# Performance work log

Hardware: AMD Instinct MI355X
Metric: run time of the kernel (lower is better)

## Reference

```python
import math
import jax, jax.numpy as jnp
import numpy as np

K = 64            # multiplicity per irrep
NE = 10           # num_elements
N_NODES = 10000
N_EDGES = 100000
AVG_NEIGH = 10.0
EDGE_DIM = 8
LS = [0, 1, 2]    # node/intermediate irreps 64x0e+64x1o+64x2e
LS_OUT = [0, 1]   # output irreps 64x0e+64x1o
INV_SQRT_K = 1.0 / math.sqrt(K)
MIX_NORM = 1.0 / math.sqrt(K * NE)

# ---- real spherical-harmonic Clebsch-Gordan coefficients (small l, exact) ----
def _cg(j1, m1, j2, m2, j3, m3):
    if m1 + m2 != m3 or not (abs(j1 - j2) <= j3 <= j1 + j2):
        return 0.0
    f = math.factorial
    pre = math.sqrt((2 * j3 + 1) * f(j1 + j2 - j3) * f(j1 - j2 + j3) * f(-j1 + j2 + j3) / f(j1 + j2 + j3 + 1))
    pre *= math.sqrt(f(j1 + m1) * f(j1 - m1) * f(j2 + m2) * f(j2 - m2) * f(j3 + m3) * f(j3 - m3))
    s = 0.0
    for k in range(j1 + j2 + j3 + 1):
        d = (j1 + j2 - j3 - k, j1 - m1 - k, j2 + m2 - k, j3 - j2 + m1 + k, j3 - j1 - m2 + k)
        if min(d) < 0:
            continue
        s += (-1) ** k / (f(k) * f(d[0]) * f(d[1]) * f(d[2]) * f(d[3]) * f(d[4]))
    return pre * s

def _u_real(l):
    # complex->real SH change of basis: Y_real = U @ Y_complex
    U = np.zeros((2 * l + 1, 2 * l + 1), dtype=np.complex128)
    U[l, l] = 1.0
    s = 1.0 / math.sqrt(2.0)
    for m in range(1, l + 1):
        U[l + m, l + m] = (-1) ** m * s
        U[l + m, l - m] = s
        U[l - m, l + m] = -1j * (-1) ** m * s
        U[l - m, l - m] = 1j * s
    return U

def real_cg(l1, l2, l3):
    C = np.zeros((2 * l1 + 1, 2 * l2 + 1, 2 * l3 + 1), dtype=np.complex128)
    for m1 in range(-l1, l1 + 1):
        for m2 in range(-l2, l2 + 1):
            m3 = m1 + m2
            if abs(m3) <= l3:
                C[l1 + m1, l2 + m2, l3 + m3] = _cg(l1, m1, l2, m2, l3, m3)
    U1, U2, U3 = _u_real(l1), _u_real(l2), _u_real(l3)
    Cr = np.einsum('ai,bj,ck,ijk->abc', U1, U2, U3.conj(), C)
    return np.ascontiguousarray(Cr.real).astype(np.float32)  # real since l1+l2+l3 even

# parity/triangle allowed paths (l1: edge sph, l2: node in, l3: intermediate) -> 11 paths
EDGE_PATHS = [(l1, l2, l3) for l1 in LS for l2 in LS for l3 in LS
              if abs(l1 - l2) <= l3 <= l1 + l2 and (l1 + l2 + l3) % 2 == 0]
N_EDGE_PATHS = len(EDGE_PATHS)  # 11
DEG2_PATHS = [(0, 0, 0), (1, 1, 0), (2, 2, 0), (0, 1, 1), (1, 2, 1)]
DEG3_PATHS = [(0, 0, 0), (1, 1, 0), (0, 1, 1), (1, 0, 1), (1, 2, 1)]
CG_EDGE = [real_cg(*p) for p in EDGE_PATHS]
CG_D2 = [real_cg(*p) for p in DEG2_PATHS]
CG_D3 = [real_cg(*p) for p in DEG3_PATHS]

def split_irreps(x, ls, mul):
    # ir_mul layout: per irrep a [(2l+1)*mul] flat segment, m index outer
    out, o = [], 0
    for l in ls:
        d = (2 * l + 1) * mul
        out.append(x[:, o:o + d].reshape(x.shape[0], 2 * l + 1, mul))
        o += d
    return out


def setup_inputs() -> dict:
    key = jax.random.key(0)
    ks = jax.random.split(key, 20)
    sender = jax.random.randint(ks[0], (N_EDGES,), 0, N_NODES)
    receiver = jax.random.randint(ks[1], (N_EDGES,), 0, N_NODES)
    indices = jax.random.randint(ks[2], (N_NODES,), 0, NE)
    node_attrs = jax.nn.one_hot(indices, NE, dtype=jnp.float32)
    node_feature_in = jax.random.normal(ks[3], (N_NODES, K * 9), dtype=jnp.float32)
    edge_length_embed = jax.random.normal(ks[4], (N_EDGES, EDGE_DIM), dtype=jnp.float32)
    edge_sph_embed = jax.random.normal(ks[5], (N_EDGES, 9), dtype=jnp.float32)
    W_lin_in = jax.random.normal(ks[6], (3, K, K), dtype=jnp.float32)
    mlp_W0 = jax.random.normal(ks[7], (EDGE_DIM, 32), dtype=jnp.float32) / math.sqrt(EDGE_DIM)
    mlp_b0 = jnp.zeros((32,), jnp.float32)
    mlp_W1 = jax.random.normal(ks[8], (32, 32), dtype=jnp.float32) / math.sqrt(32.0)
    mlp_b1 = jnp.zeros((32,), jnp.float32)
    mlp_W2 = jax.random.normal(ks[9], (32, 32), dtype=jnp.float32) / math.sqrt(32.0)
    mlp_b2 = jnp.zeros((32,), jnp.float32)
    mlp_W3 = jax.random.normal(ks[10], (32, N_EDGE_PATHS * K), dtype=jnp.float32) / math.sqrt(32.0)
    mlp_b3 = jnp.zeros((N_EDGE_PATHS * K,), jnp.float32)
    W_mix = jax.random.normal(ks[11], (3, NE, K, K), dtype=jnp.float32)
    w1 = jax.random.normal(ks[12], (NE, 2, K), dtype=jnp.float32)
    w2 = 0.1 * jax.random.normal(ks[13], (NE, len(DEG2_PATHS), K), dtype=jnp.float32)
    w3 = 0.05 * jax.random.normal(ks[14], (NE, len(DEG3_PATHS), K), dtype=jnp.float32)
    W_out_m = jax.random.normal(ks[15], (2, K, K), dtype=jnp.float32)
    W_out_h = jax.random.normal(ks[16], (2, K, K), dtype=jnp.float32)
    return dict(sender=sender, receiver=receiver, indices=indices, node_attrs=node_attrs,
                node_feature_in=node_feature_in, edge_length_embed=edge_length_embed,
                edge_sph_embed=edge_sph_embed, W_lin_in=W_lin_in,
                mlp_W0=mlp_W0, mlp_b0=mlp_b0, mlp_W1=mlp_W1, mlp_b1=mlp_b1,
                mlp_W2=mlp_W2, mlp_b2=mlp_b2, mlp_W3=mlp_W3, mlp_b3=mlp_b3,
                W_mix=W_mix, w1=w1, w2=w2, w3=w3, W_out_m=W_out_m, W_out_h=W_out_h)


def reference(sender, receiver, indices, node_attrs, node_feature_in,
              edge_length_embed, edge_sph_embed, W_lin_in,
              mlp_W0, mlp_b0, mlp_W1, mlp_b1, mlp_W2, mlp_b2, mlp_W3, mlp_b3,
              W_mix, w1, w2, w3, W_out_m, W_out_h):
    N = node_feature_in.shape[0]
    h1 = split_irreps(node_feature_in, LS, K)  # per-l [N, 2l+1, K]
    # ELinear_h1_2_h1p: per-irrep channel mixing
    h1p = [jnp.einsum('nmc,cd->nmd', h1[l], W_lin_in[l]) * INV_SQRT_K for l in LS]
    # residual radial MLP -> per-edge TP path weights [E, P, K]
    h = jax.nn.silu(edge_length_embed @ mlp_W0 + mlp_b0)
    h = h + jax.nn.silu(h @ mlp_W1 + mlp_b1)
    h = h + jax.nn.silu(h @ mlp_W2 + mlp_b2)
    Rl = (h @ mlp_W3 + mlp_b3).reshape(-1, N_EDGE_PATHS, K)
    sph = split_irreps(edge_sph_embed, LS, 1)  # per-l [E, 2l+1, 1]
    gx = [h1p[l][sender] for l in LS]          # gather sender node features
    # channelwise equivariant tensor product with per-edge radial weights
    msg = [None, None, None]
    for p, (l1, l2, l3) in enumerate(EDGE_PATHS):
        t = jnp.einsum('abd,ea,ebc->edc', jnp.asarray(CG_EDGE[p]), sph[l1][:, :, 0], gx[l2])
        t = t * Rl[:, p, None, :]
        msg[l3] = t if msg[l3] is None else msg[l3] + t
    # scatter-sum messages to receivers, normalized by avg num neighbors
    A = [jax.ops.segment_sum(msg[l], receiver, num_segments=N) / AVG_NEIGH for l in LS]
    # element-conditioned mixing (FCTP with num_elements x 0e attrs)
    Amix = [jnp.einsum('nmc,ne,ecd->nmd', A[l], node_attrs, W_mix[l]) * MIX_NORM for l in LS]
    # symmetric contraction (body order 3) with element-dependent channelwise weights
    w1n, w2n, w3n = w1[indices], w2[indices], w3[indices]
    T2 = [jnp.zeros_like(Amix[L]) for L in LS_OUT]
    for p, (l1, l2, L) in enumerate(DEG2_PATHS):
        t = jnp.einsum('abd,nac,nbc->ndc', jnp.asarray(CG_D2[p]), Amix[l1], Amix[l2])
        T2[L] = T2[L] + w2n[:, p, None, :] * t
    T3 = [jnp.zeros_like(Amix[L]) for L in LS_OUT]
    for q, (Lp, l3, L) in enumerate(DEG3_PATHS):
        t = jnp.einsum('abd,nac,nbc->ndc', jnp.asarray(CG_D3[q]), T2[Lp], Amix[l3])
        T3[L] = T3[L] + w3n[:, q, None, :] * t
    B = [w1n[:, L, None, :] * Amix[L] + T2[L] + T3[L] for L in LS_OUT]
    # node_feature_out = ELinear_h1_2_h2(h1) + ELinear_m2_2_h2(B)
    out = []
    for L in LS_OUT:
        y = jnp.einsum('nmc,cd->nmd', h1[L], W_out_h[L]) * INV_SQRT_K
        y = y + jnp.einsum('nmc,cd->nmd', B[L], W_out_m[L]) * INV_SQRT_K
        out.append(y.reshape(N, -1))
    return jnp.concatenate(out, axis=1)  # [N, 4K] = [N, 256]
```

## Files before the change

kernel.cpp:

```cpp
#include <hip/hip_runtime.h>
#include <math.h>

#define NNODES 10000
#define NEDGES 100000
#define EPW 8

struct Cplx { double re, im; };

constexpr double cfact(int n){ double r=1.0; for(int i=2;i<=n;++i) r*=i; return r; }

constexpr double csqrt_(double x){
  if (x<=0.0) return 0.0;
  double g = x<1.0 ? 1.0 : x;
  for (int it=0; it<64; ++it){ double ng = 0.5*(g + x/g); if (ng==g) break; g = ng; }
  return g;
}

constexpr double cg_coeff(int j1,int m1,int j2,int m2,int j3,int m3){
  if (m1+m2!=m3) return 0.0;
  int lo = j1>j2 ? j1-j2 : j2-j1;
  if (j3<lo || j3>j1+j2) return 0.0;
  if (m1<-j1||m1>j1||m2<-j2||m2>j2||m3<-j3||m3>j3) return 0.0;
  double pre = csqrt_((2.0*j3+1.0)*cfact(j1+j2-j3)*cfact(j1-j2+j3)*cfact(-j1+j2+j3)/cfact(j1+j2+j3+1));
  pre *= csqrt_(cfact(j1+m1)*cfact(j1-m1)*cfact(j2+m2)*cfact(j2-m2)*cfact(j3+m3)*cfact(j3-m3));
  double s = 0.0;
  for (int k=0;k<=j1+j2+j3;++k){
    int d0=j1+j2-j3-k, d1=j1-m1-k, d2=j2+m2-k, d3=j3-j2+m1+k, d4=j3-j1-m2+k;
    if (d0<0||d1<0||d2<0||d3<0||d4<0) continue;
    double term = 1.0/(cfact(k)*cfact(d0)*cfact(d1)*cfact(d2)*cfact(d3)*cfact(d4));
    s += (k&1) ? -term : term;
  }
  return pre*s;
}

constexpr Cplx uent(int l,int a,int i){
  const double s = 0.70710678118654752440;
  int ma = a - l;
  if (ma==0) { if (i==l) return Cplx{1.0,0.0}; return Cplx{0.0,0.0}; }
  if (ma>0){
    int m = ma; double sg = (m&1) ? -1.0 : 1.0;
    if (i==l+m) return Cplx{sg*s, 0.0};
    if (i==l-m) return Cplx{s, 0.0};
    return Cplx{0.0,0.0};
  }
  int m = -ma; double sg = (m&1) ? -1.0 : 1.0;
  if (i==l+m) return Cplx{0.0, -sg*s};
  if (i==l-m) return Cplx{0.0, s};
  return Cplx{0.0,0.0};
}

constexpr double real_cg_entry(int l1,int l2,int l3,int a,int b,int c){
  double acc = 0.0;
  int ii0 = a, ii1 = 2*l1-a;
  int jj0 = b, jj1 = 2*l2-b;
  for (int x=0;x<2;++x){
    int i = (x==0)? ii0 : ii1;
    if (x==1 && ii1==ii0) break;
    Cplx u1 = uent(l1,a,i); if (u1.re==0.0 && u1.im==0.0) continue;
    for (int y=0;y<2;++y){
      int j = (y==0)? jj0 : jj1;
      if (y==1 && jj1==jj0) break;
      Cplx u2 = uent(l2,b,j); if (u2.re==0.0 && u2.im==0.0) continue;
      int k = (i-l1)+(j-l2)+l3;
      if (k<0 || k>2*l3) continue;
      Cplx u3 = uent(l3,c,k); if (u3.re==0.0 && u3.im==0.0) continue;
      double cg = cg_coeff(l1,i-l1,l2,j-l2,l3,k-l3);
      if (cg==0.0) continue;
      double pr = u1.re*u2.re - u1.im*u2.im;
      double pi = u1.re*u2.im + u1.im*u2.re;
      acc += (pr*u3.re + pi*u3.im) * cg;
    }
  }
  return acc;
}

struct CGT { float v[5][5][5]; };
constexpr CGT make_cg(int l1,int l2,int l3){
  CGT t{};
  for (int a=0;a<2*l1+1;++a)
    for (int b=0;b<2*l2+1;++b)
      for (int c=0;c<2*l3+1;++c)
        t.v[a][b][c] = (float)real_cg_entry(l1,l2,l3,a,b,c);
  return t;
}

__device__ __forceinline__ float rdlane(float v, int l){
  return __int_as_float(__builtin_amdgcn_readlane(__float_as_int(v), l));
}
__device__ __forceinline__ float silu_(float x){ return x / (1.0f + __expf(-x)); }

template<int L1,int L2,int L3>
__device__ __forceinline__ void tp_accum(const float* sp, const float* g, float rl, float* msg){
  constexpr CGT T = make_cg(L1,L2,L3);
  constexpr int NA = 2*L1+1, NB = 2*L2+1, ND = 2*L3+1;
  float t[ND];
#pragma unroll
  for (int d=0; d<ND; ++d) t[d] = 0.f;
#pragma unroll
  for (int b=0;b<NB;++b){
#pragma unroll
    for (int d=0; d<ND; ++d){
      float u = 0.f; bool any = false;
#pragma unroll
      for (int a=0;a<NA;++a){
        const float cg = T.v[a][b][d];
        if (cg != 0.f){ u = fmaf(cg, sp[a], u); any = true; }
      }
      if (any) t[d] = fmaf(u, g[b], t[d]);
    }
  }
#pragma unroll
  for (int d=0;d<ND;++d) msg[d] = fmaf(rl, t[d], msg[d]);
}

template<int L1,int L2,int L3>
__device__ __forceinline__ void sc_accum(const float* X, const float* Y, float w, float* out){
  constexpr CGT T = make_cg(L1,L2,L3);
  constexpr int NA = 2*L1+1, NB = 2*L2+1, ND = 2*L3+1;
#pragma unroll
  for (int d=0;d<ND;++d){
    float s = 0.f;
#pragma unroll
    for (int a=0;a<NA;++a){
#pragma unroll
      for (int b=0;b<NB;++b){
        const float cg = T.v[a][b][d];
        if (cg != 0.f) s = fmaf(cg*X[a], Y[b], s);
      }
    }
    out[d] = fmaf(w, s, out[d]);
  }
}

__global__ void __launch_bounds__(64) k_lin_in(const float* __restrict__ h1,
                                               const float* __restrict__ W,
                                               float* __restrict__ h1p,
                                               float* __restrict__ A){
  const int n = blockIdx.x;
  const int d = threadIdx.x;
  float* Az = A + (long)n*576;
#pragma unroll
  for (int i=0;i<9;++i) Az[i*64+d] = 0.f;
  const float* row = h1 + (long)n*576;
  float acc[9];
#pragma unroll
  for (int i=0;i<9;++i) acc[i] = 0.f;
  for (int c=0;c<64;++c){
    const float w0 = W[c*64 + d];
    const float w1 = W[4096 + c*64 + d];
    const float w2 = W[8192 + c*64 + d];
    acc[0] = fmaf(row[c], w0, acc[0]);
#pragma unroll
    for (int m=0;m<3;++m) acc[1+m] = fmaf(row[64+m*64+c], w1, acc[1+m]);
#pragma unroll
    for (int m=0;m<5;++m) acc[4+m] = fmaf(row[256+m*64+c], w2, acc[4+m]);
  }
  float* o = h1p + (long)n*576;
  o[d] = acc[0]*0.125f;
#pragma unroll
  for (int m=0;m<3;++m) o[64+m*64+d] = acc[1+m]*0.125f;
#pragma unroll
  for (int m=0;m<5;++m) o[256+m*64+d] = acc[4+m]*0.125f;
}

__global__ void __launch_bounds__(256, 3) k_edge(const int* __restrict__ sender,
                                             const int* __restrict__ receiver,
                                             const float* __restrict__ ele,
                                             const float* __restrict__ sph,
                                             const float* __restrict__ h1p,
                                             const float* __restrict__ W0, const float* __restrict__ b0,
                                             const float* __restrict__ W1, const float* __restrict__ b1,
                                             const float* __restrict__ W2, const float* __restrict__ b2,
                                             const float* __restrict__ W3, const float* __restrict__ b3,
                                             float* __restrict__ A){
  __shared__ float sps[4][EPW*9];
  const int wid  = threadIdx.x >> 6;
  const int lane = threadIdx.x & 63;
  const int j32  = lane & 31;
  const long base = ((long)blockIdx.x*4 + wid) * EPW;

  sps[wid][lane < EPW*9 ? lane : 0] = sph[base*9 + (lane < EPW*9 ? lane : 0)];
  if (lane < EPW*9 - 64) sps[wid][64+lane] = sph[base*9 + 64 + lane];

  int sidx[EPW], ridx[EPW];
#pragma unroll
  for (int e=0;e<EPW;++e){ sidx[e] = sender[base+e]; ridx[e] = receiver[base+e]; }

  float g[EPW][9];
#pragma unroll
  for (int e=0;e<EPW;++e){
    const float* hp = h1p + (long)sidx[e]*576;
#pragma unroll
    for (int i=0;i<9;++i) g[e][i] = hp[i*64+lane];
  }

  float h[EPW];
#pragma unroll
  for (int e=0;e<EPW;++e){
    const float* xr = ele + (base+e)*8;
    float acc = b0[j32];
#pragma unroll
    for (int i=0;i<8;++i) acc = fmaf(xr[i], W0[i*32+j32], acc);
    h[e] = silu_(acc);
  }
#pragma unroll
  for (int L=0; L<2; ++L){
    const float* Wl = L ? W2 : W1;
    const float* bl = L ? b2 : b1;
    float acc[EPW];
#pragma unroll
    for (int e=0;e<EPW;++e) acc[e] = bl[j32];
    for (int j=0;j<32;++j){
      const float w = Wl[j*32+j32];
#pragma unroll
      for (int e=0;e<EPW;++e) acc[e] = fmaf(rdlane(h[e], j), w, acc[e]);
    }
#pragma unroll
    for (int e=0;e<EPW;++e) h[e] += silu_(acc[e]);
  }

  {
    float rl[3][EPW];
    {
      const float bb0 = b3[0*64+lane], bb4 = b3[4*64+lane], bb9 = b3[9*64+lane];
#pragma unroll
      for (int e=0;e<EPW;++e){ rl[0][e]=bb0; rl[1][e]=bb4; rl[2][e]=bb9; }
    }
    for (int j=0;j<32;++j){
      const float w_0 = W3[j*704 + 0*64 + lane];
      const float w_4 = W3[j*704 + 4*64 + lane];
      const float w_9 = W3[j*704 + 9*64 + lane];
#pragma unroll
      for (int e=0;e<EPW;++e){
        const float hj = rdlane(h[e], j);
        rl[0][e] = fmaf(hj, w_0, rl[0][e]);
        rl[1][e] = fmaf(hj, w_4, rl[1][e]);
        rl[2][e] = fmaf(hj, w_9, rl[2][e]);
      }
    }
#pragma unroll
    for (int e=0;e<EPW;++e){
      const float* sp = &sps[wid][e*9];
      float m0[1] = {0.f};
      tp_accum<0,0,0>(sp+0, &g[e][0], rl[0][e], m0);
      tp_accum<1,1,0>(sp+1, &g[e][1], rl[1][e], m0);
      tp_accum<2,2,0>(sp+4, &g[e][4], rl[2][e], m0);
      atomicAdd(&A[(long)ridx[e]*576 + lane], m0[0]);
    }
  }

#pragma unroll
  for (int e=0;e<EPW;++e)
#pragma unroll
    for (int i=0;i<9;++i) asm volatile("" : "+v"(g[e][i]));

  {
    float rl[4][EPW];
    {
      const float bb1 = b3[1*64+lane], bb3 = b3[3*64+lane], bb6 = b3[6*64+lane], bb8 = b3[8*64+lane];
#pragma unroll
      for (int e=0;e<EPW;++e){ rl[0][e]=bb1; rl[1][e]=bb3; rl[2][e]=bb6; rl[3][e]=bb8; }
    }
    for (int j=0;j<32;++j){
      const float w_1 = W3[j*704 + 1*64 + lane];
      const float w_3 = W3[j*704 + 3*64 + lane];
      const float w_6 = W3[j*704 + 6*64 + lane];
      const float w_8 = W3[j*704 + 8*64 + lane];
#pragma unroll
      for (int e=0;e<EPW;++e){
        const float hj = rdlane(h[e], j);
        rl[0][e] = fmaf(hj, w_1, rl[0][e]);
        rl[1][e] = fmaf(hj, w_3, rl[1][e]);
        rl[2][e] = fmaf(hj, w_6, rl[2][e]);
        rl[3][e] = fmaf(hj, w_8, rl[3][e]);
      }
    }
#pragma unroll
    for (int e=0;e<EPW;++e){
      const float* sp = &sps[wid][e*9];
      float m1[3] = {0.f,0.f,0.f};
      tp_accum<0,1,1>(sp+0, &g[e][1], rl[0][e], m1);
      tp_accum<1,0,1>(sp+1, &g[e][0], rl[1][e], m1);
      tp_accum<1,2,1>(sp+1, &g[e][4], rl[2][e], m1);
      tp_accum<2,1,1>(sp+4, &g[e][1], rl[3][e], m1);
#pragma unroll
      for (int m=0;m<3;++m) atomicAdd(&A[(long)ridx[e]*576 + 64 + m*64 + lane], m1[m]);
    }
  }

#pragma unroll
  for (int e=0;e<EPW;++e)
#pragma unroll
    for (int i=0;i<9;++i) asm volatile("" : "+v"(g[e][i]));

  {
    float rl[4][EPW];
    {
      const float bb2 = b3[2*64+lane], bb5 = b3[5*64+lane], bb7 = b3[7*64+lane], bb10 = b3[10*64+lane];
#pragma unroll
      for (int e=0;e<EPW;++e){ rl[0][e]=bb2; rl[1][e]=bb5; rl[2][e]=bb7; rl[3][e]=bb10; }
    }
    for (int j=0;j<32;++j){
      const float w_2  = W3[j*704 + 2*64 + lane];
      const float w_5  = W3[j*704 + 5*64 + lane];
      const float w_7  = W3[j*704 + 7*64 + lane];
      const float w_10 = W3[j*704 + 10*64 + lane];
#pragma unroll
      for (int e=0;e<EPW;++e){
        const float hj = rdlane(h[e], j);
        rl[0][e] = fmaf(hj, w_2,  rl[0][e]);
        rl[1][e] = fmaf(hj, w_5,  rl[1][e]);
        rl[2][e] = fmaf(hj, w_7,  rl[2][e]);
        rl[3][e] = fmaf(hj, w_10, rl[3][e]);
      }
    }
#pragma unroll
    for (int e=0;e<EPW;++e){
      const float* sp = &sps[wid][e*9];
      float m2[5] = {0.f,0.f,0.f,0.f,0.f};
      tp_accum<0,2,2>(sp+0, &g[e][4], rl[0][e], m2);
      tp_accum<1,1,2>(sp+1, &g[e][1], rl[1][e], m2);
      tp_accum<2,0,2>(sp+4, &g[e][0], rl[2][e], m2);
      tp_accum<2,2,2>(sp+4, &g[e][4], rl[3][e], m2);
#pragma unroll
      for (int m=0;m<5;++m) atomicAdd(&A[(long)ridx[e]*576 + 256 + m*64 + lane], m2[m]);
    }
  }
}

__global__ void __launch_bounds__(64) k_node(const int* __restrict__ indices,
                                             const float* __restrict__ h1,
                                             const float* __restrict__ A,
                                             const float* __restrict__ Wmix,
                                             const float* __restrict__ w1,
                                             const float* __restrict__ w2,
                                             const float* __restrict__ w3,
                                             const float* __restrict__ Wom,
                                             const float* __restrict__ Woh,
                                             float* __restrict__ out){
  __shared__ float Bsh[4][64];
  const int n = blockIdx.x;
  const int lane = threadIdx.x;
  const int e = indices[n];
  const float* Ar = A + (long)n*576;
  float ax[9];
#pragma unroll
  for (int i=0;i<9;++i) ax[i] = 0.f;
  {
    const float* Wm0 = Wmix + (size_t)(0*10 + e)*4096;
    const float* Wm1 = Wmix + (size_t)(1*10 + e)*4096;
    const float* Wm2 = Wmix + (size_t)(2*10 + e)*4096;
    for (int c=0;c<64;++c){
      const float wv0 = Wm0[c*64+lane];
      const float wv1 = Wm1[c*64+lane];
      const float wv2 = Wm2[c*64+lane];
      ax[0] = fmaf(Ar[c], wv0, ax[0]);
#pragma unroll
      for (int m=0;m<3;++m) ax[1+m] = fmaf(Ar[64+m*64+c], wv1, ax[1+m]);
#pragma unroll
      for (int m=0;m<5;++m) ax[4+m] = fmaf(Ar[256+m*64+c], wv2, ax[4+m]);
    }
  }
#pragma unroll
  for (int i=0;i<9;++i) ax[i] *= 0.0039528470752104741f;

  const float* amix0 = ax;
  const float* amix1 = ax+1;
  const float* amix2 = ax+4;
  float w2n[5], w3n[5];
#pragma unroll
  for (int p=0;p<5;++p){
    w2n[p] = w2[(size_t)(e*5+p)*64 + lane];
    w3n[p] = w3[(size_t)(e*5+p)*64 + lane];
  }
  float t20[1] = {0.f}, t21[3] = {0.f,0.f,0.f};
  sc_accum<0,0,0>(amix0, amix0, w2n[0], t20);
  sc_accum<1,1,0>(amix1, amix1, w2n[1], t20);
  sc_accum<2,2,0>(amix2, amix2, w2n[2], t20);
  sc_accum<0,1,1>(amix0, amix1, w2n[3], t21);
  sc_accum<1,2,1>(amix1, amix2, w2n[4], t21);
  float t30[1] = {0.f}, t31[3] = {0.f,0.f,0.f};
  sc_accum<0,0,0>(t20, amix0, w3n[0], t30);
  sc_accum<1,1,0>(t21, amix1, w3n[1], t30);
  sc_accum<0,1,1>(t20, amix1, w3n[2], t31);
  sc_accum<1,0,1>(t21, amix0, w3n[3], t31);
  sc_accum<1,2,1>(t21, amix2, w3n[4], t31);

  const float w1_0 = w1[(size_t)(e*2+0)*64 + lane];
  const float w1_1 = w1[(size_t)(e*2+1)*64 + lane];
  Bsh[0][lane] = fmaf(w1_0, amix0[0], t20[0] + t30[0]);
#pragma unroll
  for (int m=0;m<3;++m) Bsh[1+m][lane] = fmaf(w1_1, amix1[m], t21[m] + t31[m]);
  __syncthreads();

  const float* hrow = h1 + (long)n*576;
  float o[4];
#pragma unroll
  for (int i=0;i<4;++i) o[i] = 0.f;
  for (int c=0;c<64;++c){
    const float wh0 = Woh[c*64+lane];
    const float wh1 = Woh[4096 + c*64+lane];
    const float wm0 = Wom[c*64+lane];
    const float wm1 = Wom[4096 + c*64+lane];
    o[0] = fmaf(hrow[c], wh0, o[0]);
    o[0] = fmaf(Bsh[0][c], wm0, o[0]);
#pragma unroll
    for (int m=0;m<3;++m){
      o[1+m] = fmaf(hrow[64+m*64+c], wh1, o[1+m]);
      o[1+m] = fmaf(Bsh[1+m][c], wm1, o[1+m]);
    }
  }
  float* orow = out + (long)n*256;
  orow[lane] = o[0]*0.125f;
#pragma unroll
  for (int m=0;m<3;++m) orow[64+m*64+lane] = o[1+m]*0.125f;
}

extern "C" void kernel_launch(void* const* d_in, const int* in_sizes, int n_in,
                              void* d_out, int out_size, void* d_ws, size_t ws_size,
                              hipStream_t stream){
  const int*   sender   = (const int*)  d_in[0];
  const int*   receiver = (const int*)  d_in[1];
  const int*   indices  = (const int*)  d_in[2];
  const float* node_feat= (const float*)d_in[4];
  const float* ele      = (const float*)d_in[5];
  const float* sph      = (const float*)d_in[6];
  const float* W_lin    = (const float*)d_in[7];
  const float* W0 = (const float*)d_in[8],  *b0 = (const float*)d_in[9];
  const float* W1 = (const float*)d_in[10], *b1 = (const float*)d_in[11];
  const float* W2 = (const float*)d_in[12], *b2 = (const float*)d_in[13];
  const float* W3 = (const float*)d_in[14], *b3 = (const float*)d_in[15];
  const float* Wmix = (const float*)d_in[16];
  const float* w1 = (const float*)d_in[17];
  const float* w2 = (const float*)d_in[18];
  const float* w3 = (const float*)d_in[19];
  const float* Wom = (const float*)d_in[20];
  const float* Woh = (const float*)d_in[21];
  float* out = (float*)d_out;

  float* h1p = (float*)d_ws;
  float* A   = h1p + (size_t)NNODES*576;

  k_lin_in<<<NNODES, 64, 0, stream>>>(node_feat, W_lin, h1p, A);
  k_edge<<<NEDGES/(4*EPW), 256, 0, stream>>>(sender, receiver, ele, sph, h1p,
                                             W0,b0,W1,b1,W2,b2,W3,b3, A);
  k_node<<<NNODES, 64, 0, stream>>>(indices, node_feat, A, Wmix, w1, w2, w3, Wom, Woh, out);
}
```

Measured before the change: 306.5 us.

## Split the radial MLP into its own kernel and read hidden states via scalar loads

The first three radial MLP layers move out of the edge kernel into a separate per-edge thread kernel that writes a 32-wide hidden vector per edge to workspace. The edge kernel then reads those values with wave-uniform (readfirstlane-based) addresses instead of doing the MLP with 32-lane readlane broadcasts, and batches W3 loads in groups of 8. This removes readlane chains and half-idle lanes from the edge kernel. In exchange it adds an extra launch and a 12.8 MB write and read round trip, and relies on the compiler turning the hidden-state reads into scalar loads.

```diff
diff --git a/kernel.cpp b/kernel.cpp
--- a/kernel.cpp
+++ b/kernel.cpp
@@ -84,9 +84,6 @@
   return t;
 }
 
-__device__ __forceinline__ float rdlane(float v, int l){
-  return __int_as_float(__builtin_amdgcn_readlane(__float_as_int(v), l));
-}
 __device__ __forceinline__ float silu_(float x){ return x / (1.0f + __expf(-x)); }
 
 template<int L1,int L2,int L3>
@@ -163,28 +160,62 @@
   for (int m=0;m<5;++m) o[256+m*64+d] = acc[4+m]*0.125f;
 }
 
-__global__ void __launch_bounds__(256, 3) k_edge(const int* __restrict__ sender,
-                                             const int* __restrict__ receiver,
-                                             const float* __restrict__ ele,
-                                             const float* __restrict__ sph,
-                                             const float* __restrict__ h1p,
+__global__ void __launch_bounds__(256) k_mlp(const float* __restrict__ ele,
                                              const float* __restrict__ W0, const float* __restrict__ b0,
                                              const float* __restrict__ W1, const float* __restrict__ b1,
                                              const float* __restrict__ W2, const float* __restrict__ b2,
+                                             float* __restrict__ hmlp){
+  const int e = blockIdx.x*256 + threadIdx.x;
+  if (e >= NEDGES) return;
+  float x[8];
+#pragma unroll
+  for (int i=0;i<8;++i) x[i] = ele[(long)e*8 + i];
+  float h[32];
+#pragma unroll
+  for (int d=0;d<32;++d){
+    float acc = b0[d];
+#pragma unroll
+    for (int i=0;i<8;++i) acc = fmaf(x[i], W0[i*32+d], acc);
+    h[d] = silu_(acc);
+  }
+#pragma unroll
+  for (int L=0; L<2; ++L){
+    const float* Wl = L ? W2 : W1;
+    const float* bl = L ? b2 : b1;
+    float acc[32];
+#pragma unroll
+    for (int d=0;d<32;++d) acc[d] = bl[d];
+    for (int j=0;j<32;++j){
+      const float hj = h[j];
+#pragma unroll
+      for (int d=0;d<32;++d) acc[d] = fmaf(hj, Wl[j*32+d], acc[d]);
+    }
+#pragma unroll
+    for (int d=0;d<32;++d) h[d] += silu_(acc[d]);
+  }
+  float* o = hmlp + (long)e*32;
+#pragma unroll
+  for (int d=0;d<32;++d) o[d] = h[d];
+}
+
+__global__ void __launch_bounds__(256, 3) k_edge(const int* __restrict__ sender,
+                                             const int* __restrict__ receiver,
+                                             const float* __restrict__ hmlp,
+                                             const float* __restrict__ sph,
+                                             const float* __restrict__ h1p,
                                              const float* __restrict__ W3, const float* __restrict__ b3,
                                              float* __restrict__ A){
   __shared__ float sps[4][EPW*9];
   const int wid  = threadIdx.x >> 6;
   const int lane = threadIdx.x & 63;
-  const int j32  = lane & 31;
-  const long base = ((long)blockIdx.x*4 + wid) * EPW;
-
-  sps[wid][lane < EPW*9 ? lane : 0] = sph[base*9 + (lane < EPW*9 ? lane : 0)];
-  if (lane < EPW*9 - 64) sps[wid][64+lane] = sph[base*9 + 64 + lane];
+  const int ubase = __builtin_amdgcn_readfirstlane((blockIdx.x*4 + wid) * EPW);
+
+  sps[wid][lane < EPW*9 ? lane : 0] = sph[(long)ubase*9 + (lane < EPW*9 ? lane : 0)];
+  if (lane < EPW*9 - 64) sps[wid][64+lane] = sph[(long)ubase*9 + 64 + lane];
 
   int sidx[EPW], ridx[EPW];
 #pragma unroll
-  for (int e=0;e<EPW;++e){ sidx[e] = sender[base+e]; ridx[e] = receiver[base+e]; }
+  for (int e=0;e<EPW;++e){ sidx[e] = sender[ubase+e]; ridx[e] = receiver[ubase+e]; }
 
   float g[EPW][9];
 #pragma unroll
@@ -194,30 +225,7 @@
     for (int i=0;i<9;++i) g[e][i] = hp[i*64+lane];
   }
 
-  float h[EPW];
-#pragma unroll
-  for (int e=0;e<EPW;++e){
-    const float* xr = ele + (base+e)*8;
-    float acc = b0[j32];
-#pragma unroll
-    for (int i=0;i<8;++i) acc = fmaf(xr[i], W0[i*32+j32], acc);
-    h[e] = silu_(acc);
-  }
-#pragma unroll
-  for (int L=0; L<2; ++L){
-    const float* Wl = L ? W2 : W1;
-    const float* bl = L ? b2 : b1;
-    float acc[EPW];
-#pragma unroll
-    for (int e=0;e<EPW;++e) acc[e] = bl[j32];
-    for (int j=0;j<32;++j){
-      const float w = Wl[j*32+j32];
-#pragma unroll
-      for (int e=0;e<EPW;++e) acc[e] = fmaf(rdlane(h[e], j), w, acc[e]);
-    }
-#pragma unroll
-    for (int e=0;e<EPW;++e) h[e] += silu_(acc[e]);
-  }
+  const float* hu = hmlp + (long)ubase*32;
 
   {
     float rl[3][EPW];
@@ -226,16 +234,23 @@
 #pragma unroll
       for (int e=0;e<EPW;++e){ rl[0][e]=bb0; rl[1][e]=bb4; rl[2][e]=bb9; }
     }
-    for (int j=0;j<32;++j){
-      const float w_0 = W3[j*704 + 0*64 + lane];
-      const float w_4 = W3[j*704 + 4*64 + lane];
-      const float w_9 = W3[j*704 + 9*64 + lane];
+    for (int jb=0;jb<32;jb+=8){
+      float w3v[8][3];
+#pragma unroll
+      for (int jj=0;jj<8;++jj){
+        w3v[jj][0] = W3[(jb+jj)*704 + 0*64 + lane];
+        w3v[jj][1] = W3[(jb+jj)*704 + 4*64 + lane];
+        w3v[jj][2] = W3[(jb+jj)*704 + 9*64 + lane];
+      }
 #pragma unroll
       for (int e=0;e<EPW;++e){
-        const float hj = rdlane(h[e], j);
-        rl[0][e] = fmaf(hj, w_0, rl[0][e]);
-        rl[1][e] = fmaf(hj, w_4, rl[1][e]);
-        rl[2][e] = fmaf(hj, w_9, rl[2][e]);
+#pragma unroll
+        for (int jj=0;jj<8;++jj){
+          const float hj = hu[e*32 + jb + jj];
+          rl[0][e] = fmaf(hj, w3v[jj][0], rl[0][e]);
+          rl[1][e] = fmaf(hj, w3v[jj][1], rl[1][e]);
+          rl[2][e] = fmaf(hj, w3v[jj][2], rl[2][e]);
+        }
       }
     }
 #pragma unroll
@@ -261,18 +276,25 @@
 #pragma unroll
       for (int e=0;e<EPW;++e){ rl[0][e]=bb1; rl[1][e]=bb3; rl[2][e]=bb6; rl[3][e]=bb8; }
     }
-    for (int j=0;j<32;++j){
-      const float w_1 = W3[j*704 + 1*64 + lane];
-      const float w_3 = W3[j*704 + 3*64 + lane];
-      const float w_6 = W3[j*704 + 6*64 + lane];
-      const float w_8 = W3[j*704 + 8*64 + lane];
+    for (int jb=0;jb<32;jb+=8){
+      float w3v[8][4];
+#pragma unroll
+      for (int jj=0;jj<8;++jj){
+        w3v[jj][0] = W3[(jb+jj)*704 + 1*64 + lane];
+        w3v[jj][1] = W3[(jb+jj)*704 + 3*64 + lane];
+        w3v[jj][2] = W3[(jb+jj)*704 + 6*64 + lane];
+        w3v[jj][3] = W3[(jb+jj)*704 + 8*64 + lane];
+      }
 #pragma unroll
       for (int e=0;e<EPW;++e){
-        const float hj = rdlane(h[e], j);
-        rl[0][e] = fmaf(hj, w_1, rl[0][e]);
-        rl[1][e] = fmaf(hj, w_3, rl[1][e]);
-        rl[2][e] = fmaf(hj, w_6, rl[2][e]);
-        rl[3][e] = fmaf(hj, w_8, rl[3][e]);
+#pragma unroll
+        for (int jj=0;jj<8;++jj){
+          const float hj = hu[e*32 + jb + jj];
+          rl[0][e] = fmaf(hj, w3v[jj][0], rl[0][e]);
+          rl[1][e] = fmaf(hj, w3v[jj][1], rl[1][e]);
+          rl[2][e] = fmaf(hj, w3v[jj][2], rl[2][e]);
+          rl[3][e] = fmaf(hj, w3v[jj][3], rl[3][e]);
+        }
       }
     }
 #pragma unroll
@@ -300,18 +322,25 @@
 #pragma unroll
       for (int e=0;e<EPW;++e){ rl[0][e]=bb2; rl[1][e]=bb5; rl[2][e]=bb7; rl[3][e]=bb10; }
     }
-    for (int j=0;j<32;++j){
-      const float w_2  = W3[j*704 + 2*64 + lane];
-      const float w_5  = W3[j*704 + 5*64 + lane];
-      const float w_7  = W3[j*704 + 7*64 + lane];
-      const float w_10 = W3[j*704 + 10*64 + lane];
+    for (int jb=0;jb<32;jb+=8){
+      float w3v[8][4];
+#pragma unroll
+      for (int jj=0;jj<8;++jj){
+        w3v[jj][0] = W3[(jb+jj)*704 + 2*64 + lane];
+        w3v[jj][1] = W3[(jb+jj)*704 + 5*64 + lane];
+        w3v[jj][2] = W3[(jb+jj)*704 + 7*64 + lane];
+        w3v[jj][3] = W3[(jb+jj)*704 + 10*64 + lane];
+      }
 #pragma unroll
       for (int e=0;e<EPW;++e){
-        const float hj = rdlane(h[e], j);
-        rl[0][e] = fmaf(hj, w_2,  rl[0][e]);
-        rl[1][e] = fmaf(hj, w_5,  rl[1][e]);
-        rl[2][e] = fmaf(hj, w_7,  rl[2][e]);
-        rl[3][e] = fmaf(hj, w_10, rl[3][e]);
+#pragma unroll
+        for (int jj=0;jj<8;++jj){
+          const float hj = hu[e*32 + jb + jj];
+          rl[0][e] = fmaf(hj, w3v[jj][0], rl[0][e]);
+          rl[1][e] = fmaf(hj, w3v[jj][1], rl[1][e]);
+          rl[2][e] = fmaf(hj, w3v[jj][2], rl[2][e]);
+          rl[3][e] = fmaf(hj, w3v[jj][3], rl[3][e]);
+        }
       }
     }
 #pragma unroll
@@ -438,11 +467,13 @@
   const float* Woh = (const float*)d_in[21];
   float* out = (float*)d_out;
 
-  float* h1p = (float*)d_ws;
-  float* A   = h1p + (size_t)NNODES*576;
+  float* h1p  = (float*)d_ws;
+  float* A    = h1p + (size_t)NNODES*576;
+  float* hmlp = A + (size_t)NNODES*576;
 
   k_lin_in<<<NNODES, 64, 0, stream>>>(node_feat, W_lin, h1p, A);
-  k_edge<<<NEDGES/(4*EPW), 256, 0, stream>>>(sender, receiver, ele, sph, h1p,
-                                             W0,b0,W1,b1,W2,b2,W3,b3, A);
+  k_mlp<<<(NEDGES+255)/256, 256, 0, stream>>>(ele, W0,b0,W1,b1,W2,b2, hmlp);
+  k_edge<<<NEDGES/(4*EPW), 256, 0, stream>>>(sender, receiver, hmlp, sph, h1p,
+                                             W3, b3, A);
   k_node<<<NNODES, 64, 0, stream>>>(indices, node_feat, A, Wmix, w1, w2, w3, Wom, Woh, out);
 }
```

After: 320.8 us. 4.7% more time.
